# Optimization experiments

Hardware: AMD Instinct MI355X
Metric: run time of the kernel (lower is better)

The kernel has to match this reference:

```python
import jax, jax.numpy as jnp
import numpy as np

NUM_HEADS = 8
NG = 8  # group/grid size: seq = NG**3 = 512


def setup_inputs() -> dict:
    key = jax.random.key(0)
    k1, k2, k3 = jax.random.split(key, 3)
    batch, seq, chan = 32, NG ** 3, 512
    subspace_dim = 24
    x = jax.random.normal(k1, (batch, seq, chan), jnp.float32)
    # fixed symmetric-subspace basis (the free variable `conv_kernel` in the source)
    basis = jax.random.normal(k2, (seq, subspace_dim), jnp.float32)
    # learned param: (subspace_dim, num_heads), init stddev 0.01
    kernel = jax.random.normal(k3, (subspace_dim, NUM_HEADS), jnp.float32) * 0.01
    return {"x": x, "basis": basis, "kernel": kernel}


def reference(x, basis, kernel):
    batch, seq, chan = x.shape
    h, ng = NUM_HEADS, NG
    kn = 2 * ng - 1  # 15: circular tiling window
    ch = chan // h
    # 'batch (8 8 8) (ch h) -> h (batch ch) 8 8 8'
    x_im = x.reshape(batch, ng, ng, ng, ch, h)
    x_im = jnp.transpose(x_im, (5, 0, 4, 1, 2, 3)).reshape(h, batch * ch, ng, ng, ng)
    # circular tiling: tile 2x2x2 then crop to 2*ng-1 per axis; add trailing C=1
    x_im = jnp.tile(x_im, (1, 1, 2, 2, 2))[:, :, :kn, :kn, :kn, None]
    # expand subspace kernel: '(n n n) s, s h -> h n n n 1 1'
    kexp = jnp.einsum('gs,sh->hg', basis, kernel).reshape(h, ng, ng, ng, 1, 1)

    def conv(lhs, rhs):
        return jax.lax.conv_general_dilated(
            lhs, rhs, window_strides=(1, 1, 1), padding='VALID',
            dimension_numbers=('NXYZC', 'XYZIO', 'NXYZC'))

    # per-head VALID conv: [batch*ch, 15,15,15, 1] * [8,8,8,1,1] -> [batch*ch, 8,8,8, 1]
    out = jax.vmap(conv)(x_im, kexp)[..., 0]  # [h, batch*ch, 8, 8, 8]
    # 'h (batch ch) n n n -> batch (n n n) (ch h)'
    out = out.reshape(h, batch, ch, seq)
    out = jnp.transpose(out, (1, 3, 2, 0)).reshape(batch, seq, chan)
    return out
```

## Files before the change

kernel.cpp:

```cpp
#include <hip/hip_runtime.h>


#define S2C 0.70710678118654752f
#define S2  18
#define S1  146
#define CST 1172

template <bool INV>
__device__ __forceinline__ void dft8(float* R, float* I)
{
    float t0r = R[0] + R[4], t0i = I[0] + I[4];
    float t1r = R[1] + R[5], t1i = I[1] + I[5];
    float t2r = R[2] + R[6], t2i = I[2] + I[6];
    float t3r = R[3] + R[7], t3i = I[3] + I[7];
    float b0r = R[0] - R[4], b0i = I[0] - I[4];
    float d1r = R[1] - R[5], d1i = I[1] - I[5];
    float d2r = R[2] - R[6], d2i = I[2] - I[6];
    float d3r = R[3] - R[7], d3i = I[3] - I[7];
    float b1r, b1i, b2r, b2i, b3r, b3i;
    if (!INV) {
        b1r = (d1r + d1i) * S2C;  b1i = (d1i - d1r) * S2C;
        b2r = d2i;                b2i = -d2r;
        b3r = (d3i - d3r) * S2C;  b3i = -(d3r + d3i) * S2C;
    } else {
        b1r = (d1r - d1i) * S2C;  b1i = (d1i + d1r) * S2C;
        b2r = -d2i;               b2i = d2r;
        b3r = -(d3r + d3i) * S2C; b3i = (d3r - d3i) * S2C;
    }
    float u0r = t0r + t2r, u0i = t0i + t2i;
    float u1r = t1r + t3r, u1i = t1i + t3i;
    float u2r = t0r - t2r, u2i = t0i - t2i;
    float e3r = t1r - t3r, e3i = t1i - t3i;
    float u3r, u3i;
    if (!INV) { u3r = e3i;  u3i = -e3r; }
    else      { u3r = -e3i; u3i = e3r;  }
    R[0] = u0r + u1r; I[0] = u0i + u1i;
    R[4] = u0r - u1r; I[4] = u0i - u1i;
    R[2] = u2r + u3r; I[2] = u2i + u3i;
    R[6] = u2r - u3r; I[6] = u2i - u3i;
    float v0r = b0r + b2r, v0i = b0i + b2i;
    float v1r = b1r + b3r, v1i = b1i + b3i;
    float v2r = b0r - b2r, v2i = b0i - b2i;
    float w3r = b1r - b3r, w3i = b1i - b3i;
    float v3r, v3i;
    if (!INV) { v3r = w3i;  v3i = -w3r; }
    else      { v3r = -w3i; v3i = w3r;  }
    R[1] = v0r + v1r; I[1] = v0i + v1i;
    R[5] = v0r - v1r; I[5] = v0i - v1i;
    R[3] = v2r + v3r; I[3] = v2i + v3i;
    R[7] = v2r - v3r; I[7] = v2i - v3i;
}

template <int HB, int LM>
__device__ __forceinline__ void xstage(float* zr, float* zi, int lane)
{
    const bool sel = (lane & LM) != 0;
    #pragma unroll
    for (int j0 = 0; j0 < 8; ++j0) {
        if (j0 & HB) continue;
        const int j1 = j0 | HB;
        float sr = sel ? zr[j0] : zr[j1];
        float si = sel ? zi[j0] : zi[j1];
        sr = __shfl_xor(sr, LM, 64);
        si = __shfl_xor(si, LM, 64);
        zr[j0] = sel ? sr : zr[j0];
        zi[j0] = sel ? si : zi[j0];
        zr[j1] = sel ? zr[j1] : sr;
        zi[j1] = sel ? zi[j1] : si;
    }
}

__device__ const float CTAB8[8] = {1.f, S2C, 0.f, -S2C, -1.f, -S2C, 0.f, S2C};
__device__ const float STAB8[8] = {0.f, S2C, 1.f, S2C, 0.f, -S2C, -1.f, -S2C};

__global__ __launch_bounds__(256)
void eqfft_prep(const float* __restrict__ basis,
                const float* __restrict__ kparam,
                float2* __restrict__ V)
{
    __shared__ float Wl[512];
    __shared__ float CT[8], ST[8];
    const int tid = threadIdx.x;
    const int blk = blockIdx.x;
    const int h   = blk >> 4;
    if (tid < 8) { CT[tid] = CTAB8[tid]; ST[tid] = STAB8[tid]; }
    #pragma unroll
    for (int t = 0; t < 2; ++t) {
        const int g = tid * 2 + t;
        const float* bp = basis + g * 24;
        float acc = 0.f;
        #pragma unroll
        for (int s = 0; s < 24; ++s) acc += bp[s] * kparam[s * 8 + h];
        Wl[(g & 63) * 8 + (g >> 6)] = acc;
    }
    __syncthreads();
    const int f  = (blk & 15) * 32 + (tid >> 3);
    const int g1 = tid & 7;
    const int f1 = f >> 6, f2 = (f >> 3) & 7, f3 = f & 7;
    const int kb = (f1 * g1) & 7;
    float pr = 0.f, pi = 0.f;
    for (int g2 = 0; g2 < 8; ++g2) {
        const int k2 = kb + f2 * g2;
        const float* wrow = &Wl[g2 * 64 + g1];
        #pragma unroll
        for (int g3 = 0; g3 < 8; ++g3) {
            const int k = (k2 + f3 * g3) & 7;
            const float w = wrow[g3 * 8];
            pr += w * CT[k];
            pi += w * ST[k];
        }
    }
    pr += __shfl_xor(pr, 1); pi += __shfl_xor(pi, 1);
    pr += __shfl_xor(pr, 2); pi += __shfl_xor(pi, 2);
    pr += __shfl_xor(pr, 4); pi += __shfl_xor(pi, 4);
    if (g1 == 0)
        V[h * 512 + f] = make_float2(pr * (1.f / 512.f), pi * (1.f / 512.f));
}

__global__ __launch_bounds__(256, 4)
void eqfft_main(const float* __restrict__ x,
                const float2* __restrict__ V,
                float* __restrict__ out)
{
    __shared__ __align__(16) float lds[8 * CST];

    const int tid = threadIdx.x;
    const int bid = blockIdx.x;
    const int b   = bid >> 5;
    const int c0  = (bid & 31) * 16;

    const float* xb = x   + (size_t)b * 262144 + c0;
    float*       ob = out + (size_t)b * 262144 + c0;

    #pragma unroll
    for (int t = 0; t < 4; ++t) {
        const int G = t * 256 + tid;
        const int p = G >> 1;
        const int u = G & 1;
        const float4 A  = *(const float4*)(xb + p * 512 + u * 4);
        const float4 Bv = *(const float4*)(xb + p * 512 + u * 4 + 8);
        const int base = (p >> 6) * S1 + ((p >> 3) & 7) * S2 + (p & 7) * 2;
        float* dst = lds + (u * 4) * CST + base;
        *(float2*)(dst + 0 * CST) = make_float2(A.x, Bv.x);
        *(float2*)(dst + 1 * CST) = make_float2(A.y, Bv.y);
        *(float2*)(dst + 2 * CST) = make_float2(A.z, Bv.z);
        *(float2*)(dst + 3 * CST) = make_float2(A.w, Bv.w);
    }
    __syncthreads();

    const int lane = tid & 63;
    const int wid  = tid >> 6;

    #pragma unroll
    for (int cc = 0; cc < 2; ++cc) {
        const int q = wid * 2 + cc;
        float zr[8], zi[8];
        float* pp = lds + q * CST + (lane >> 3) * S1 + (lane & 7) * S2;
        #pragma unroll
        for (int j = 0; j < 8; ++j) {
            const float2 z = *(const float2*)(pp + 2 * j);
            zr[j] = z.x; zi[j] = z.y;
        }
        dft8<false>(zr, zi);
        xstage<1, 1>(zr, zi, lane);
        xstage<2, 2>(zr, zi, lane);
        xstage<4, 4>(zr, zi, lane);
        dft8<false>(zr, zi);
        xstage<1, 8>(zr, zi, lane);
        xstage<2, 16>(zr, zi, lane);
        xstage<4, 32>(zr, zi, lane);
        dft8<false>(zr, zi);
        const float2* vp = V + q * 512 + lane;
        #pragma unroll
        for (int j = 0; j < 8; ++j) {
            const float2 v = vp[j * 64];
            const float nr = zr[j] * v.x - zi[j] * v.y;
            zi[j] = zr[j] * v.y + zi[j] * v.x;
            zr[j] = nr;
        }
        dft8<true>(zr, zi);
        xstage<1, 8>(zr, zi, lane);
        xstage<2, 16>(zr, zi, lane);
        xstage<4, 32>(zr, zi, lane);
        dft8<true>(zr, zi);
        xstage<1, 1>(zr, zi, lane);
        xstage<2, 2>(zr, zi, lane);
        xstage<4, 4>(zr, zi, lane);
        dft8<true>(zr, zi);
        #pragma unroll
        for (int j = 0; j < 8; ++j)
            *(float2*)(pp + 2 * j) = make_float2(zr[j], zi[j]);
    }
    __syncthreads();

    #pragma unroll
    for (int t = 0; t < 4; ++t) {
        const int G = t * 256 + tid;
        const int p = G >> 1;
        const int u = G & 1;
        const int base = (p >> 6) * S1 + ((p >> 3) & 7) * S2 + (p & 7) * 2;
        const float* src = lds + (u * 4) * CST + base;
        const float2 z0 = *(const float2*)(src + 0 * CST);
        const float2 z1 = *(const float2*)(src + 1 * CST);
        const float2 z2 = *(const float2*)(src + 2 * CST);
        const float2 z3 = *(const float2*)(src + 3 * CST);
        *(float4*)(ob + p * 512 + u * 4)     = make_float4(z0.x, z1.x, z2.x, z3.x);
        *(float4*)(ob + p * 512 + u * 4 + 8) = make_float4(z0.y, z1.y, z2.y, z3.y);
    }
}

extern "C" void kernel_launch(void* const* d_in, const int* in_sizes, int n_in,
                              void* d_out, int out_size, void* d_ws, size_t ws_size,
                              hipStream_t stream)
{
    const float* x      = (const float*)d_in[0];
    const float* basis  = (const float*)d_in[1];
    const float* kparam = (const float*)d_in[2];
    float* out          = (float*)d_out;
    float2* V           = (float2*)d_ws;

    hipLaunchKernelGGL(eqfft_prep, dim3(128),  dim3(256), 0, stream, basis, kparam, V);
    hipLaunchKernelGGL(eqfft_main, dim3(1024), dim3(256), 0, stream, x, V, out);
}
```

Before: 112.9 us.

## Replace shuffle-based FFT transposes with XOR-swizzled LDS passes per axis

The 3D FFT axis transposes, previously done with cross-lane shuffles in registers, now go through shared memory. Each axis pass reads eight points along that axis from an XOR-swizzled unpadded LDS layout to avoid bank conflicts, and each wave handles two channels together for more instruction-level parallelism. Padding is removed so the LDS footprint shrinks, and the occupancy hint rises to 5 blocks per CU. Correctness relies on a wave-local fence (waitcnt plus sched barrier) between passes, which assumes each wave only touches its own channels.

```diff
diff --git a/kernel.cpp b/kernel.cpp
--- a/kernel.cpp
+++ b/kernel.cpp
@@ -2,9 +2,12 @@
 
 
 #define S2C 0.70710678118654752f
-#define S2  18
-#define S1  146
-#define CST 1172
+
+__device__ __forceinline__ void wave_fence()
+{
+    asm volatile("s_waitcnt lgkmcnt(0)" ::: "memory");
+    __builtin_amdgcn_sched_barrier(0);
+}
 
 template <bool INV>
 __device__ __forceinline__ void dft8(float* R, float* I)
@@ -51,25 +54,6 @@
     R[7] = v2r - v3r; I[7] = v2i - v3i;
 }
 
-template <int HB, int LM>
-__device__ __forceinline__ void xstage(float* zr, float* zi, int lane)
-{
-    const bool sel = (lane & LM) != 0;
-    #pragma unroll
-    for (int j0 = 0; j0 < 8; ++j0) {
-        if (j0 & HB) continue;
-        const int j1 = j0 | HB;
-        float sr = sel ? zr[j0] : zr[j1];
-        float si = sel ? zi[j0] : zi[j1];
-        sr = __shfl_xor(sr, LM, 64);
-        si = __shfl_xor(si, LM, 64);
-        zr[j0] = sel ? sr : zr[j0];
-        zi[j0] = sel ? si : zi[j0];
-        zr[j1] = sel ? zr[j1] : sr;
-        zi[j1] = sel ? zi[j1] : si;
-    }
-}
-
 __device__ const float CTAB8[8] = {1.f, S2C, 0.f, -S2C, -1.f, -S2C, 0.f, S2C};
 __device__ const float STAB8[8] = {0.f, S2C, 1.f, S2C, 0.f, -S2C, -1.f, -S2C};
 
@@ -117,12 +101,12 @@
         V[h * 512 + f] = make_float2(pr * (1.f / 512.f), pi * (1.f / 512.f));
 }
 
-__global__ __launch_bounds__(256, 4)
+__global__ __launch_bounds__(256, 5)
 void eqfft_main(const float* __restrict__ x,
                 const float2* __restrict__ V,
                 float* __restrict__ out)
 {
-    __shared__ __align__(16) float lds[8 * CST];
+    __shared__ float2 lds[8 * 512];
 
     const int tid = threadIdx.x;
     const int bid = blockIdx.x;
@@ -139,57 +123,112 @@
         const int u = G & 1;
         const float4 A  = *(const float4*)(xb + p * 512 + u * 4);
         const float4 Bv = *(const float4*)(xb + p * 512 + u * 4 + 8);
-        const int base = (p >> 6) * S1 + ((p >> 3) & 7) * S2 + (p & 7) * 2;
-        float* dst = lds + (u * 4) * CST + base;
-        *(float2*)(dst + 0 * CST) = make_float2(A.x, Bv.x);
-        *(float2*)(dst + 1 * CST) = make_float2(A.y, Bv.y);
-        *(float2*)(dst + 2 * CST) = make_float2(A.z, Bv.z);
-        *(float2*)(dst + 3 * CST) = make_float2(A.w, Bv.w);
+        const int p1 = p >> 6, p2 = (p >> 3) & 7, p3 = p & 7;
+        const int s  = p1 * 64 + p2 * 8 + (p3 ^ p2 ^ p1);
+        float2* dst = lds + (u * 4) * 512 + s;
+        dst[0 * 512] = make_float2(A.x, Bv.x);
+        dst[1 * 512] = make_float2(A.y, Bv.y);
+        dst[2 * 512] = make_float2(A.z, Bv.z);
+        dst[3 * 512] = make_float2(A.w, Bv.w);
     }
     __syncthreads();
 
     const int lane = tid & 63;
     const int wid  = tid >> 6;
-
-    #pragma unroll
-    for (int cc = 0; cc < 2; ++cc) {
-        const int q = wid * 2 + cc;
-        float zr[8], zi[8];
-        float* pp = lds + q * CST + (lane >> 3) * S1 + (lane & 7) * S2;
+    const int q0   = wid * 2;
+    const int hi3  = lane >> 3, lo3 = lane & 7;
+    const int xs   = lo3 ^ hi3;
+
+    float r0[8], i0[8], r1[8], i1[8];
+
+    {
+        float2* c0p = lds + q0 * 512 + hi3 * 64 + lo3 * 8;
+        float2* c1p = c0p + 512;
+        #pragma unroll
+        for (int j = 0; j < 8; ++j) { const float2 z = c0p[xs ^ j]; r0[j] = z.x; i0[j] = z.y; }
+        #pragma unroll
+        for (int j = 0; j < 8; ++j) { const float2 z = c1p[xs ^ j]; r1[j] = z.x; i1[j] = z.y; }
+        dft8<false>(r0, i0); dft8<false>(r1, i1);
+        #pragma unroll
+        for (int j = 0; j < 8; ++j) c0p[xs ^ j] = make_float2(r0[j], i0[j]);
+        #pragma unroll
+        for (int j = 0; j < 8; ++j) c1p[xs ^ j] = make_float2(r1[j], i1[j]);
+    }
+    wave_fence();
+
+    {
+        float2* c0p = lds + q0 * 512 + hi3 * 64;
+        float2* c1p = c0p + 512;
+        #pragma unroll
+        for (int j = 0; j < 8; ++j) { const float2 z = c0p[j * 8 + (xs ^ j)]; r0[j] = z.x; i0[j] = z.y; }
+        #pragma unroll
+        for (int j = 0; j < 8; ++j) { const float2 z = c1p[j * 8 + (xs ^ j)]; r1[j] = z.x; i1[j] = z.y; }
+        dft8<false>(r0, i0); dft8<false>(r1, i1);
+        #pragma unroll
+        for (int j = 0; j < 8; ++j) c0p[j * 8 + (xs ^ j)] = make_float2(r0[j], i0[j]);
+        #pragma unroll
+        for (int j = 0; j < 8; ++j) c1p[j * 8 + (xs ^ j)] = make_float2(r1[j], i1[j]);
+    }
+    wave_fence();
+
+    {
+        const float2* v0 = V + q0 * 512 + lane;
+        const float2* v1 = v0 + 512;
+        float2 va[8], vb[8];
+        #pragma unroll
+        for (int j = 0; j < 8; ++j) { va[j] = v0[j * 64]; vb[j] = v1[j * 64]; }
+
+        float2* c0p = lds + q0 * 512 + hi3 * 8;
+        float2* c1p = c0p + 512;
+        #pragma unroll
+        for (int j = 0; j < 8; ++j) { const float2 z = c0p[j * 64 + (xs ^ j)]; r0[j] = z.x; i0[j] = z.y; }
+        #pragma unroll
+        for (int j = 0; j < 8; ++j) { const float2 z = c1p[j * 64 + (xs ^ j)]; r1[j] = z.x; i1[j] = z.y; }
+        dft8<false>(r0, i0); dft8<false>(r1, i1);
         #pragma unroll
         for (int j = 0; j < 8; ++j) {
-            const float2 z = *(const float2*)(pp + 2 * j);
-            zr[j] = z.x; zi[j] = z.y;
+            float nr = r0[j] * va[j].x - i0[j] * va[j].y;
+            i0[j]    = r0[j] * va[j].y + i0[j] * va[j].x;
+            r0[j]    = nr;
+            nr       = r1[j] * vb[j].x - i1[j] * vb[j].y;
+            i1[j]    = r1[j] * vb[j].y + i1[j] * vb[j].x;
+            r1[j]    = nr;
         }
-        dft8<false>(zr, zi);
-        xstage<1, 1>(zr, zi, lane);
-        xstage<2, 2>(zr, zi, lane);
-        xstage<4, 4>(zr, zi, lane);
-        dft8<false>(zr, zi);
-        xstage<1, 8>(zr, zi, lane);
-        xstage<2, 16>(zr, zi, lane);
-        xstage<4, 32>(zr, zi, lane);
-        dft8<false>(zr, zi);
-        const float2* vp = V + q * 512 + lane;
-        #pragma unroll
-        for (int j = 0; j < 8; ++j) {
-            const float2 v = vp[j * 64];
-            const float nr = zr[j] * v.x - zi[j] * v.y;
-            zi[j] = zr[j] * v.y + zi[j] * v.x;
-            zr[j] = nr;
-        }
-        dft8<true>(zr, zi);
-        xstage<1, 8>(zr, zi, lane);
-        xstage<2, 16>(zr, zi, lane);
-        xstage<4, 32>(zr, zi, lane);
-        dft8<true>(zr, zi);
-        xstage<1, 1>(zr, zi, lane);
-        xstage<2, 2>(zr, zi, lane);
-        xstage<4, 4>(zr, zi, lane);
-        dft8<true>(zr, zi);
-        #pragma unroll
-        for (int j = 0; j < 8; ++j)
-            *(float2*)(pp + 2 * j) = make_float2(zr[j], zi[j]);
+        dft8<true>(r0, i0); dft8<true>(r1, i1);
+        #pragma unroll
+        for (int j = 0; j < 8; ++j) c0p[j * 64 + (xs ^ j)] = make_float2(r0[j], i0[j]);
+        #pragma unroll
+        for (int j = 0; j < 8; ++j) c1p[j * 64 + (xs ^ j)] = make_float2(r1[j], i1[j]);
+    }
+    wave_fence();
+
+    {
+        float2* c0p = lds + q0 * 512 + hi3 * 64;
+        float2* c1p = c0p + 512;
+        #pragma unroll
+        for (int j = 0; j < 8; ++j) { const float2 z = c0p[j * 8 + (xs ^ j)]; r0[j] = z.x; i0[j] = z.y; }
+        #pragma unroll
+        for (int j = 0; j < 8; ++j) { const float2 z = c1p[j * 8 + (xs ^ j)]; r1[j] = z.x; i1[j] = z.y; }
+        dft8<true>(r0, i0); dft8<true>(r1, i1);
+        #pragma unroll
+        for (int j = 0; j < 8; ++j) c0p[j * 8 + (xs ^ j)] = make_float2(r0[j], i0[j]);
+        #pragma unroll
+        for (int j = 0; j < 8; ++j) c1p[j * 8 + (xs ^ j)] = make_float2(r1[j], i1[j]);
+    }
+    wave_fence();
+
+    {
+        float2* c0p = lds + q0 * 512 + hi3 * 64 + lo3 * 8;
+        float2* c1p = c0p + 512;
+        #pragma unroll
+        for (int j = 0; j < 8; ++j) { const float2 z = c0p[xs ^ j]; r0[j] = z.x; i0[j] = z.y; }
+        #pragma unroll
+        for (int j = 0; j < 8; ++j) { const float2 z = c1p[xs ^ j]; r1[j] = z.x; i1[j] = z.y; }
+        dft8<true>(r0, i0); dft8<true>(r1, i1);
+        #pragma unroll
+        for (int j = 0; j < 8; ++j) c0p[xs ^ j] = make_float2(r0[j], i0[j]);
+        #pragma unroll
+        for (int j = 0; j < 8; ++j) c1p[xs ^ j] = make_float2(r1[j], i1[j]);
     }
     __syncthreads();
 
@@ -198,12 +237,13 @@
         const int G = t * 256 + tid;
         const int p = G >> 1;
         const int u = G & 1;
-        const int base = (p >> 6) * S1 + ((p >> 3) & 7) * S2 + (p & 7) * 2;
-        const float* src = lds + (u * 4) * CST + base;
-        const float2 z0 = *(const float2*)(src + 0 * CST);
-        const float2 z1 = *(const float2*)(src + 1 * CST);
-        const float2 z2 = *(const float2*)(src + 2 * CST);
-        const float2 z3 = *(const float2*)(src + 3 * CST);
+        const int p1 = p >> 6, p2 = (p >> 3) & 7, p3 = p & 7;
+        const int s  = p1 * 64 + p2 * 8 + (p3 ^ p2 ^ p1);
+        const float2* src = lds + (u * 4) * 512 + s;
+        const float2 z0 = src[0 * 512];
+        const float2 z1 = src[1 * 512];
+        const float2 z2 = src[2 * 512];
+        const float2 z3 = src[3 * 512];
         *(float4*)(ob + p * 512 + u * 4)     = make_float4(z0.x, z1.x, z2.x, z3.x);
         *(float4*)(ob + p * 512 + u * 4 + 8) = make_float4(z0.y, z1.y, z2.y, z3.y);
     }
```

Result: faster. 106.5 us (-5.7%).
